# Optimization experiments

Measured on AMD Instinct MI355X. Metric: run time of the kernel, lower is better.

The kernel has to match this reference:

```python
import jax, jax.numpy as jnp
import numpy as np

MARGIN = 0.2  # TripletMarginLoss margin and TripletMarginMiner margin


def setup_inputs() -> dict:
    key = jax.random.key(0)
    k1, k2 = jax.random.split(key)
    embeddings = jax.random.normal(k1, (384, 256), dtype=jnp.float32)
    labels = jax.random.randint(k2, (384,), 0, 32)
    return {"embeddings": embeddings, "labels": labels}


def _pairwise_l2(e):
    # Euclidean distance matrix with sqrt-safe gradient at zero.
    sq = jnp.sum(e * e, axis=1)
    d2 = jnp.maximum(sq[:, None] + sq[None, :] - 2.0 * (e @ e.T), 0.0)
    pos = d2 > 0.0
    return jnp.sqrt(jnp.where(pos, d2, 1.0)) * pos


def reference(embeddings, labels):
    # pytorch-metric-learning LpDistance defaults: normalize_embeddings=True, p=2
    e = embeddings / jnp.maximum(
        jnp.linalg.norm(embeddings, axis=1, keepdims=True), 1e-12
    )
    D = _pairwise_l2(e)  # [B, B]
    n = D.shape[0]

    same = labels[:, None] == labels[None, :]
    eye = jnp.eye(n, dtype=bool)
    pos_mask = same & ~eye   # valid (anchor, positive) pairs
    neg_mask = ~same         # valid (anchor, negative) pairs

    ap = D[:, :, None]       # dist(anchor, positive), broadcast over negative
    an = D[:, None, :]       # dist(anchor, negative), broadcast over positive
    tm = an - ap             # miner's triplet_margin (is_inverted=False)

    valid = pos_mask[:, :, None] & neg_mask[:, None, :]     # [B, B, B]
    # semihard miner: 0 < an - ap <= margin
    semihard = valid & (tm > 0.0) & (tm <= MARGIN)

    # TripletMarginLoss per-triplet loss: relu(ap - an + margin) = relu(margin - tm)
    losses = jnp.where(semihard, jnp.maximum(MARGIN - tm, 0.0), 0.0)

    # AvgNonZeroReducer: mean over strictly-positive losses (0 if none)
    nz = jnp.sum(losses > 0.0)
    total = jnp.sum(losses)
    return jnp.where(nz > 0, total / jnp.maximum(nz, 1).astype(total.dtype), 0.0)
```

## Files before the change

kernel.cpp:

```cpp
#include <hip/hip_runtime.h>

#define N        384
#define DIM      256
#define D4       (DIM / 4)
#define KH       (D4 / 2)
#define MARGIN_F 0.2f
#define NANCH    2
#define NBLK     (N / NANCH)
#define NTHR     (2 * N)
#define NWAVE    (NTHR / 64)
#define MAXPOS   64


__global__ __launch_bounds__(64) void norm_kernel(
    const float* __restrict__ emb, float4* __restrict__ eTv,
    float* __restrict__ sqn)
{
    const int row  = blockIdx.x;
    const int lane = threadIdx.x;

    const float4 v = ((const float4*)emb)[row * D4 + lane];
    float s = v.x*v.x + v.y*v.y + v.z*v.z + v.w*v.w;
    #pragma unroll
    for (int off = 32; off > 0; off >>= 1) s += __shfl_down(s, off, 64);
    const float tot = __shfl(s, 0, 64);

    const float inv = 1.0f / fmaxf(sqrtf(tot), 1e-12f);
    float4 vn;
    vn.x = v.x * inv; vn.y = v.y * inv; vn.z = v.z * inv; vn.w = v.w * inv;
    eTv[lane * N + row] = vn;

    if (lane == 0) sqn[row] = tot * inv * inv;
}

__global__ __launch_bounds__(NTHR) void fused_kernel(
    const float4* __restrict__ eTv, const float* __restrict__ sqn,
    const int* __restrict__ labels,
    float* __restrict__ accum_sum, unsigned int* __restrict__ accum_cnt,
    unsigned int* __restrict__ done_cnt, float* __restrict__ out)
{
    const int i0   = blockIdx.x * NANCH;
    const int tid  = threadIdx.x;
    const int wave = tid >> 6, lane = tid & 63;
    const int kgrp = (tid >= N) ? 1 : 0;
    const int col  = tid - kgrp * N;

    __shared__ float4 ei4[NANCH][D4];
    __shared__ float  sqa[NANCH];
    __shared__ float  pacc[NANCH][N];
    __shared__ float  Drow[NANCH][N];
    __shared__ int    lab[N];
    __shared__ int    posList[NANCH][MAXPOS];
    __shared__ int    posCnt[NANCH];
    __shared__ float        sredS[NWAVE];
    __shared__ unsigned int sredC[NWAVE];

    if (tid < NANCH * D4) {
        const int a = tid >> 6, k4 = tid & (D4 - 1);
        ei4[a][k4] = eTv[k4 * N + (i0 + a)];
    }
    if (tid < NANCH) { sqa[tid] = sqn[i0 + tid]; posCnt[tid] = 0; }
    if (tid < N) lab[tid] = labels[tid];
    __syncthreads();

    float acc0 = 0.0f, acc1 = 0.0f;
    const int kbase = kgrp * KH;
    #pragma unroll 8
    for (int k = 0; k < KH; ++k) {
        const int k4 = kbase + k;
        const float4 v  = eTv[k4 * N + col];
        const float4 a0 = ei4[0][k4];
        const float4 a1 = ei4[1][k4];
        acc0 += v.x*a0.x + v.y*a0.y + v.z*a0.z + v.w*a0.w;
        acc1 += v.x*a1.x + v.y*a1.y + v.z*a1.z + v.w*a1.w;
    }
    if (kgrp == 1) { pacc[0][col] = acc0; pacc[1][col] = acc1; }
    __syncthreads();

    if (kgrp == 0) {
        acc0 += pacc[0][col];
        acc1 += pacc[1][col];
        const float sqj = sqn[col];
        float d2 = fmaxf(sqa[0] + sqj - 2.0f * acc0, 0.0f);
        Drow[0][col] = (d2 > 0.0f) ? sqrtf(d2) : 0.0f;
        d2       = fmaxf(sqa[1] + sqj - 2.0f * acc1, 0.0f);
        Drow[1][col] = (d2 > 0.0f) ? sqrtf(d2) : 0.0f;
    } else {
        const int lj = lab[col];
        #pragma unroll
        for (int a = 0; a < NANCH; ++a) {
            const int ia = i0 + a;
            if (lj == lab[ia] && col != ia)
                posList[a][atomicAdd(&posCnt[a], 1)] = col;
        }
    }
    __syncthreads();

    float        lsum = 0.0f;
    unsigned int lcnt = 0u;
    {
        const int   a  = kgrp;
        const int   li = lab[i0 + a];
        if (lab[col] != li) {
            const float dk = Drow[a][col];
            const int   np = posCnt[a];
            for (int p = 0; p < np; ++p) {
                const float tm = dk - Drow[a][posList[a][p]];
                if (tm > 0.0f && tm <= MARGIN_F) {
                    const float l = MARGIN_F - tm;
                    lsum += l;
                    if (l > 0.0f) lcnt++;
                }
            }
        }
    }

    #pragma unroll
    for (int off = 32; off > 0; off >>= 1) {
        lsum += __shfl_down(lsum, off, 64);
        lcnt += __shfl_down(lcnt, off, 64);
    }
    if (lane == 0) { sredS[wave] = lsum; sredC[wave] = lcnt; }
    __syncthreads();

    if (tid == 0) {
        float        S = 0.0f;
        unsigned int C = 0u;
        #pragma unroll
        for (int w = 0; w < NWAVE; ++w) { S += sredS[w]; C += sredC[w]; }
        if (S != 0.0f || C != 0u) {
            atomicAdd(accum_sum, S);
            atomicAdd(accum_cnt, C);
        }
        __threadfence();
        const unsigned int prev = atomicAdd(done_cnt, 1);
        if (prev == NBLK - 1) {
            const float        Sall = atomicAdd(accum_sum, 0.0f);
            const unsigned int Call = atomicAdd(accum_cnt, 0u);
            out[0] = (Call > 0u) ? (Sall / (float)Call) : 0.0f;
        }
    }
}

extern "C" void kernel_launch(void* const* d_in, const int* in_sizes, int n_in,
                              void* d_out, int out_size, void* d_ws, size_t ws_size,
                              hipStream_t stream) {
    const float* emb    = (const float*)d_in[0];
    const int*   labels = (const int*)d_in[1];
    float*       out    = (float*)d_out;

    float*        accum_sum = (float*)d_ws;
    unsigned int* accum_cnt = (unsigned int*)accum_sum + 1;
    unsigned int* done_cnt  = (unsigned int*)accum_sum + 2;
    float4*       eTv = (float4*)((char*)d_ws + 16);
    float*        sqn = (float*)((char*)d_ws + 16 + (size_t)N * DIM * 4);

    hipMemsetAsync(d_ws, 0, 16, stream);
    norm_kernel<<<N, 64, 0, stream>>>(emb, eTv, sqn);
    fused_kernel<<<NBLK, NTHR, 0, stream>>>(eTv, sqn, labels,
                                            accum_sum, accum_cnt, done_cnt, out);
}
```

Before: 74.74 us.

## Fuse normalization into triplet kernel, staging raw embeddings through LDS chunks

Drops the separate normalize/transpose kernel. Each block now reads raw row-major embeddings and stages 8-float4 chunks into padded shared memory for coalesced loads. Row norms are computed on the fly and applied to the dot products afterwards. This removes one launch and the transposed workspace round-trip, at the cost of every block recomputing all norms, more shared memory (about 110KB, which limits occupancy) and extra barriers per chunk.

Measured after the change: 73.10 us, median of 2. 1.02x faster.

```diff
diff --git a/kernel.cpp b/kernel.cpp
--- a/kernel.cpp
+++ b/kernel.cpp
@@ -3,39 +3,19 @@
 #define N        384
 #define DIM      256
 #define D4       (DIM / 4)
-#define KH       (D4 / 2)
+#define CHUNK_K4 8
+#define NCHUNK   4
 #define MARGIN_F 0.2f
 #define NANCH    2
 #define NBLK     (N / NANCH)
 #define NTHR     (2 * N)
 #define NWAVE    (NTHR / 64)
 #define MAXPOS   64
+#define LROW     (CHUNK_K4 + 1)
 
 
-__global__ __launch_bounds__(64) void norm_kernel(
-    const float* __restrict__ emb, float4* __restrict__ eTv,
-    float* __restrict__ sqn)
-{
-    const int row  = blockIdx.x;
-    const int lane = threadIdx.x;
-
-    const float4 v = ((const float4*)emb)[row * D4 + lane];
-    float s = v.x*v.x + v.y*v.y + v.z*v.z + v.w*v.w;
-    #pragma unroll
-    for (int off = 32; off > 0; off >>= 1) s += __shfl_down(s, off, 64);
-    const float tot = __shfl(s, 0, 64);
-
-    const float inv = 1.0f / fmaxf(sqrtf(tot), 1e-12f);
-    float4 vn;
-    vn.x = v.x * inv; vn.y = v.y * inv; vn.z = v.z * inv; vn.w = v.w * inv;
-    eTv[lane * N + row] = vn;
-
-    if (lane == 0) sqn[row] = tot * inv * inv;
-}
-
-__global__ __launch_bounds__(NTHR) void fused_kernel(
-    const float4* __restrict__ eTv, const float* __restrict__ sqn,
-    const int* __restrict__ labels,
+__global__ __launch_bounds__(NTHR) void triplet_kernel(
+    const float4* __restrict__ emb4, const int* __restrict__ labels,
     float* __restrict__ accum_sum, unsigned int* __restrict__ accum_cnt,
     unsigned int* __restrict__ done_cnt, float* __restrict__ out)
 {
@@ -45,46 +25,55 @@
     const int kgrp = (tid >= N) ? 1 : 0;
     const int col  = tid - kgrp * N;
 
-    __shared__ float4 ei4[NANCH][D4];
-    __shared__ float  sqa[NANCH];
-    __shared__ float  pacc[NANCH][N];
+    __shared__ float4 ebuf[2][N][LROW];
+    __shared__ float  pacc[3][N];
     __shared__ float  Drow[NANCH][N];
+    __shared__ float  invA[NANCH], sqA[NANCH];
     __shared__ int    lab[N];
     __shared__ int    posList[NANCH][MAXPOS];
     __shared__ int    posCnt[NANCH];
     __shared__ float        sredS[NWAVE];
     __shared__ unsigned int sredC[NWAVE];
 
-    if (tid < NANCH * D4) {
-        const int a = tid >> 6, k4 = tid & (D4 - 1);
-        ei4[a][k4] = eTv[k4 * N + (i0 + a)];
+    if (tid < N) lab[tid] = labels[tid];
+    if (tid < NANCH) posCnt[tid] = 0;
+
+    float vv = 0.0f, rd0 = 0.0f, rd1 = 0.0f;
+    const int kbase = kgrp * (NCHUNK * CHUNK_K4);
+
+    for (int c = 0; c < NCHUNK; ++c) {
+        const int kk0 = kbase + c * CHUNK_K4;
+        #pragma unroll
+        for (int i = 0; i < 8; ++i) {
+            const int s   = i * N + col;
+            const int row = s >> 3, j = s & 7;
+            ebuf[kgrp][row][j] = emb4[row * D4 + kk0 + j];
+        }
+        __syncthreads();
+        #pragma unroll
+        for (int j = 0; j < CHUNK_K4; ++j) {
+            const float4 v  = ebuf[kgrp][col][j];
+            const float4 a0 = ebuf[kgrp][i0][j];
+            const float4 a1 = ebuf[kgrp][i0 + 1][j];
+            vv  += v.x*v.x  + v.y*v.y  + v.z*v.z  + v.w*v.w;
+            rd0 += v.x*a0.x + v.y*a0.y + v.z*a0.z + v.w*a0.w;
+            rd1 += v.x*a1.x + v.y*a1.y + v.z*a1.z + v.w*a1.w;
+        }
+        __syncthreads();
     }
-    if (tid < NANCH) { sqa[tid] = sqn[i0 + tid]; posCnt[tid] = 0; }
-    if (tid < N) lab[tid] = labels[tid];
+
+    if (kgrp == 1) { pacc[0][col] = vv; pacc[1][col] = rd0; pacc[2][col] = rd1; }
     __syncthreads();
 
-    float acc0 = 0.0f, acc1 = 0.0f;
-    const int kbase = kgrp * KH;
-    #pragma unroll 8
-    for (int k = 0; k < KH; ++k) {
-        const int k4 = kbase + k;
-        const float4 v  = eTv[k4 * N + col];
-        const float4 a0 = ei4[0][k4];
-        const float4 a1 = ei4[1][k4];
-        acc0 += v.x*a0.x + v.y*a0.y + v.z*a0.z + v.w*a0.w;
-        acc1 += v.x*a1.x + v.y*a1.y + v.z*a1.z + v.w*a1.w;
-    }
-    if (kgrp == 1) { pacc[0][col] = acc0; pacc[1][col] = acc1; }
-    __syncthreads();
-
+    float inv_j = 0.0f, sq_j = 0.0f;
     if (kgrp == 0) {
-        acc0 += pacc[0][col];
-        acc1 += pacc[1][col];
-        const float sqj = sqn[col];
-        float d2 = fmaxf(sqa[0] + sqj - 2.0f * acc0, 0.0f);
-        Drow[0][col] = (d2 > 0.0f) ? sqrtf(d2) : 0.0f;
-        d2       = fmaxf(sqa[1] + sqj - 2.0f * acc1, 0.0f);
-        Drow[1][col] = (d2 > 0.0f) ? sqrtf(d2) : 0.0f;
+        vv  += pacc[0][col];
+        rd0 += pacc[1][col];
+        rd1 += pacc[2][col];
+        inv_j = 1.0f / fmaxf(sqrtf(vv), 1e-12f);
+        sq_j  = vv * inv_j * inv_j;
+        if (col == i0)     { invA[0] = inv_j; sqA[0] = sq_j; }
+        if (col == i0 + 1) { invA[1] = inv_j; sqA[1] = sq_j; }
     } else {
         const int lj = lab[col];
         #pragma unroll
@@ -96,11 +85,19 @@
     }
     __syncthreads();
 
+    if (kgrp == 0) {
+        float d2 = fmaxf(sqA[0] + sq_j - 2.0f * (rd0 * (invA[0] * inv_j)), 0.0f);
+        Drow[0][col] = (d2 > 0.0f) ? sqrtf(d2) : 0.0f;
+        d2       = fmaxf(sqA[1] + sq_j - 2.0f * (rd1 * (invA[1] * inv_j)), 0.0f);
+        Drow[1][col] = (d2 > 0.0f) ? sqrtf(d2) : 0.0f;
+    }
+    __syncthreads();
+
     float        lsum = 0.0f;
     unsigned int lcnt = 0u;
     {
-        const int   a  = kgrp;
-        const int   li = lab[i0 + a];
+        const int a  = kgrp;
+        const int li = lab[i0 + a];
         if (lab[col] != li) {
             const float dk = Drow[a][col];
             const int   np = posCnt[a];
@@ -145,18 +142,15 @@
 extern "C" void kernel_launch(void* const* d_in, const int* in_sizes, int n_in,
                               void* d_out, int out_size, void* d_ws, size_t ws_size,
                               hipStream_t stream) {
-    const float* emb    = (const float*)d_in[0];
-    const int*   labels = (const int*)d_in[1];
-    float*       out    = (float*)d_out;
+    const float4* emb4   = (const float4*)d_in[0];
+    const int*    labels = (const int*)d_in[1];
+    float*        out    = (float*)d_out;
 
     float*        accum_sum = (float*)d_ws;
     unsigned int* accum_cnt = (unsigned int*)accum_sum + 1;
     unsigned int* done_cnt  = (unsigned int*)accum_sum + 2;
-    float4*       eTv = (float4*)((char*)d_ws + 16);
-    float*        sqn = (float*)((char*)d_ws + 16 + (size_t)N * DIM * 4);
 
     hipMemsetAsync(d_ws, 0, 16, stream);
-    norm_kernel<<<N, 64, 0, stream>>>(emb, eTv, sqn);
-    fused_kernel<<<NBLK, NTHR, 0, stream>>>(eTv, sqn, labels,
-                                            accum_sum, accum_cnt, done_cnt, out);
+    triplet_kernel<<<NBLK, NTHR, 0, stream>>>(emb4, labels,
+                                              accum_sum, accum_cnt, done_cnt, out);
 }
```
